# Optimization experiments

Hardware: AMD Instinct MI355X
Metric: run time of the kernel (lower is better)

Reference implementation:

```python
import jax, jax.numpy as jnp
import numpy as np

IN_FEATS = 64
ONSET = 0.8
CUTOFF = 1.0
N_NODES = 100000
N_EDGES = 1600000


def smooth_cutoff(d):
    # 1 below onset, 0 above cutoff, smooth cosine ramp in between
    x = (d - ONSET) / (CUTOFF - ONSET)
    ramp = 0.5 * (jnp.cos(jnp.pi * jnp.clip(x, 0.0, 1.0)) + 1.0)
    return jnp.where(d <= ONSET, 1.0, jnp.where(d >= CUTOFF, 0.0, ramp))


def setup_inputs() -> dict:
    key = jax.random.key(0)
    ks = jax.random.split(key, 8)
    h = jax.random.normal(ks[0], (N_NODES, IN_FEATS), dtype=jnp.float32)
    dist = jax.random.uniform(ks[1], (N_EDGES,), dtype=jnp.float32)
    W1 = jax.random.normal(ks[2], (IN_FEATS, IN_FEATS), dtype=jnp.float32) / jnp.sqrt(IN_FEATS)
    b1 = jnp.zeros((IN_FEATS,), dtype=jnp.float32)
    W2 = jax.random.normal(ks[3], (IN_FEATS, IN_FEATS), dtype=jnp.float32) / jnp.sqrt(IN_FEATS)
    b2 = jnp.zeros((IN_FEATS,), dtype=jnp.float32)
    src_idx = jax.random.randint(ks[4], (N_EDGES,), 0, N_NODES, dtype=jnp.int64 if jax.config.jax_enable_x64 else jnp.int32).astype(jnp.int32)
    dst_idx = jax.random.randint(ks[5], (N_EDGES,), 0, N_NODES, dtype=jnp.int32)
    return {"h": h, "dist": dist, "W1": W1, "b1": b1, "W2": W2, "b2": b2,
            "src_idx": src_idx, "dst_idx": dst_idx}


def reference(h, dist, W1, b1, W2, b2, src_idx, dst_idx):
    gamma = jnp.float32(IN_FEATS / (CUTOFF - 0.0))  # in_feats / (range hi - lo)
    muk = jnp.linspace(0.0, CUTOFF, IN_FEATS, dtype=jnp.float32)  # [K]
    # per-edge RBF basis: [E, K]
    rbf = jnp.exp(-gamma * (dist[:, None] - muk[None, :]) ** 2)
    fcut = smooth_cutoff(dist)[:, None]  # [E, 1]
    msg = h[src_idx] * rbf * fcut  # gather src feats, [E, K]
    agg = jax.ops.segment_sum(msg, dst_idx, num_segments=N_NODES)  # [N, K]
    # MLP: Linear -> softplus -> Linear
    hid = jax.nn.softplus(agg @ W1 + b1)
    out = hid @ W2 + b2
    return out
```

## Files before the change

kernel.cpp:

```cpp
#include <hip/hip_runtime.h>
#include <hip/hip_fp16.h>
#include <math.h>

#define IN_FEATS 64
#define N_NODES 100000
#define N_EDGES 1600000
#define BSHIFT 7
#define NPB 128
#define NBUCK ((N_NODES + NPB - 1) / NPB)
#define CAP 4088
#define PCHUNK 8192
#define PGRID ((N_EDGES + PCHUNK - 1) / PCHUNK)
#define NGRP (N_NODES / 16)

#define KSCALE 9.6089785f

typedef __attribute__((ext_vector_type(8))) short short8_t;
typedef __attribute__((ext_vector_type(4))) float f32x4_t;

#define MFMA16(a, b, c) __builtin_amdgcn_mfma_f32_16x16x32_bf16(a, b, c, 0, 0, 0)

__device__ __forceinline__ unsigned short bf16_rne(float x) {
    unsigned u = __float_as_uint(x);
    unsigned r = u + 0x7FFFu + ((u >> 16) & 1u);
    return (unsigned short)(r >> 16);
}

__device__ __forceinline__ short8_t u4_to_s8(uint4 v) {
    union { uint4 u; short8_t s; } cv; cv.u = v; return cv.s;
}

__device__ __forceinline__ void split8(float4 a, float4 b,
                                       short8_t* hi, short8_t* lo) {
    float x0 = a.x, x1 = a.y, x2 = a.z, x3 = a.w;
    float x4 = b.x, x5 = b.y, x6 = b.z, x7 = b.w;
    short8_t h, l;
#define SP(I, X) { unsigned short hu = bf16_rne(X); \
        float hf = __uint_as_float((unsigned)hu << 16); \
        unsigned short lu = bf16_rne((X) - hf); \
        h[I] = (short)hu; l[I] = (short)lu; }
    SP(0, x0) SP(1, x1) SP(2, x2) SP(3, x3)
    SP(4, x4) SP(5, x5) SP(6, x6) SP(7, x7)
#undef SP
    *hi = h; *lo = l;
}

__device__ __forceinline__ float edge_coef(float d, float mu) {
    float t = d - mu;
    float rbf = __expf(-64.0f * t * t);
    float x  = (d - 0.8f) * 5.0f;
    float xc = fminf(fmaxf(x, 0.0f), 1.0f);
    float ramp = 0.5f * (__cosf(3.14159265358979323846f * xc) + 1.0f);
    float fc = (d <= 0.8f) ? 1.0f : ((d >= 1.0f) ? 0.0f : ramp);
    return rbf * fc;
}

__device__ __forceinline__ float cutoff_fc(float d) {
    float x  = (d - 0.8f) * 5.0f;
    float xc = fminf(fmaxf(x, 0.0f), 1.0f);
    float ramp = 0.5f * (__cosf(3.14159265358979323846f * xc) + 1.0f);
    return (d <= 0.8f) ? 1.0f : ((d >= 1.0f) ? 0.0f : ramp);
}

__global__ __launch_bounds__(256) void init_kernel(int* __restrict__ bcursor,
                                                   int* __restrict__ offs,
                                                   const float* __restrict__ W1,
                                                   const float* __restrict__ W2,
                                                   uint4* __restrict__ wfrag) {
    int i = blockIdx.x * 256 + threadIdx.x;
    if (i < NBUCK) bcursor[i] = i * CAP;
    if (i == 0) offs[N_NODES] = N_EDGES;
    if (i < 2048) {
        int lane  = i & 63;
        int tile  = (i >> 6) & 7;
        int hl    = (i >> 9) & 1;
        int layer = (i >> 10) & 1;
        const float* W = layer ? W2 : W1;
        int kbase = (tile >> 2) * 32 + (lane >> 4) * 8;
        int j     = (tile & 3) * 16 + (lane & 15);
        unsigned p[4];
        #pragma unroll
        for (int e = 0; e < 8; e += 2) {
            float x0 = W[(kbase + e) * 64 + j];
            float x1 = W[(kbase + e + 1) * 64 + j];
            unsigned short u0, u1;
            if (hl == 0) {
                u0 = bf16_rne(x0);
                u1 = bf16_rne(x1);
            } else {
                unsigned short h0 = bf16_rne(x0);
                unsigned short h1 = bf16_rne(x1);
                u0 = bf16_rne(x0 - __uint_as_float((unsigned)h0 << 16));
                u1 = bf16_rne(x1 - __uint_as_float((unsigned)h1 << 16));
            }
            p[e >> 1] = (unsigned)u0 | ((unsigned)u1 << 16);
        }
        wfrag[i] = make_uint4(p[0], p[1], p[2], p[3]);
    }
}

__global__ __launch_bounds__(1024) void partition_kernel(const int* __restrict__ dst,
                                                         const int* __restrict__ src,
                                                         const float* __restrict__ dist,
                                                         int* __restrict__ bcursor,
                                                         int2* __restrict__ brec) {
    __shared__ int hist[NBUCK];
    __shared__ int base_[NBUCK];
    int tid = threadIdx.x;
    for (int i = tid; i < NBUCK; i += 1024) hist[i] = 0;
    __syncthreads();

    int e0 = blockIdx.x * PCHUNK;
    int e1 = min(e0 + PCHUNK, N_EDGES);

    for (int t = e0 + tid; t < e1; t += 1024)
        atomicAdd(&hist[dst[t] >> BSHIFT], 1);
    __syncthreads();

    for (int i = tid; i < NBUCK; i += 1024) {
        int hv = hist[i];
        if (hv) base_[i] = atomicAdd(&bcursor[i], hv);
        hist[i] = 0;
    }
    __syncthreads();

    for (int t = e0 + tid; t < e1; t += 1024) {
        int d  = dst[t];
        int b  = d >> BSHIFT;
        int r  = atomicAdd(&hist[b], 1);
        float dv = dist[t];
        float fc = cutoff_fc(dv);
        float lfc = (fc > 0.0f) ? __log2f(fc) : -512.0f;
        unsigned dq = (unsigned)(fminf(fmaxf(dv, 0.0f), 1.0f) * 65535.0f + 0.5f);
        unsigned hf = (unsigned)__half_as_ushort(__float2half(lfc));
        int2 rec;
        rec.x = src[t] | ((d & (NPB - 1)) << 17);
        rec.y = (int)((hf << 16) | dq);
        brec[(size_t)base_[b] + r] = rec;
    }
}

__global__ __launch_bounds__(1024) void bscan_kernel(const int* __restrict__ bcursor,
                                                     int* __restrict__ boffs) {
    __shared__ int lds[1024];
    int tid = threadIdx.x;
    int v = (tid < NBUCK) ? (bcursor[tid] - tid * CAP) : 0;
    lds[tid] = v;
    __syncthreads();
    for (int off = 1; off < 1024; off <<= 1) {
        int x = (tid >= off) ? lds[tid - off] : 0;
        __syncthreads();
        lds[tid] += x;
        __syncthreads();
    }
    if (tid < NBUCK) boffs[tid] = lds[tid] - v;
    if (tid == 0) boffs[NBUCK] = N_EDGES;
}

__global__ __launch_bounds__(256) void node_sort_kernel(const int2* __restrict__ brec,
                                                        const int* __restrict__ boffs,
                                                        int2* __restrict__ rec_sorted,
                                                        int* __restrict__ offs) {
    __shared__ int cntL[NPB];
    __shared__ int scanL[NPB];
    __shared__ int curL[NPB];

    int b   = blockIdx.x;
    int tid = threadIdx.x;
    int beg = boffs[b];
    int cnt = boffs[b + 1] - beg;
    size_t pbase = (size_t)b * CAP;
    int node0 = b << BSHIFT;

    for (int i = tid; i < NPB; i += 256) cntL[i] = 0;
    __syncthreads();

    for (int t = tid; t < cnt; t += 256)
        atomicAdd(&cntL[(brec[pbase + t].x >> 17) & (NPB - 1)], 1);
    __syncthreads();

    if (tid < NPB) scanL[tid] = cntL[tid];
    __syncthreads();
    for (int off = 1; off < NPB; off <<= 1) {
        int x = 0;
        if (tid < NPB && tid >= off) x = scanL[tid - off];
        __syncthreads();
        if (tid < NPB) scanL[tid] += x;
        __syncthreads();
    }
    if (tid < NPB) {
        int excl = scanL[tid] - cntL[tid];
        curL[tid] = excl;
        int node = node0 + tid;
        if (node < N_NODES) offs[node] = beg + excl;
    }
    __syncthreads();

    for (int t = tid; t < cnt; t += 256) {
        int2 r = brec[pbase + t];
        int dl = (r.x >> 17) & (NPB - 1);
        int p  = atomicAdd(&curL[dl], 1);
        rec_sorted[(size_t)beg + p] = r;
    }
}

__global__ __launch_bounds__(256) void agg_kernel(
    const float* __restrict__ h,
    const int* __restrict__ offs,
    const int2* __restrict__ rec_sorted,
    float* __restrict__ out)
{
    int w    = threadIdx.x >> 6;
    int lane = threadIdx.x & 63;
    int node = blockIdx.x * 4 + w;
    if (node >= N_NODES) return;

    int beg = __builtin_amdgcn_readfirstlane(offs[node]);
    int end = __builtin_amdgcn_readfirstlane(offs[node + 1]);
    float muK = (float)lane * (KSCALE / 63.0f);
    float acc0 = 0.0f, acc1 = 0.0f;

#define REC(J, ACC) { \
        int2 r_ = rec_sorted[(size_t)(J)]; \
        int rx_ = __builtin_amdgcn_readfirstlane(r_.x); \
        unsigned ry_ = (unsigned)__builtin_amdgcn_readfirstlane(r_.y); \
        float hv_ = h[((size_t)(rx_ & 0x1FFFF) << 6) + lane]; \
        float dqf_ = (float)(ry_ & 0xFFFFu); \
        float lfc_ = __half2float(__ushort_as_half((unsigned short)(ry_ >> 16))); \
        float t_  = fmaf(dqf_, (KSCALE / 65535.0f), -muK); \
        float a_  = fmaf(-t_, t_, lfc_); \
        ACC = fmaf(hv_, exp2f(a_), ACC); }

    int i = beg;
    int main_end = beg + ((end - beg) & ~7);
    for (; i < main_end; i += 8) {
        REC(i + 0, acc0) REC(i + 1, acc1) REC(i + 2, acc0) REC(i + 3, acc1)
        REC(i + 4, acc0) REC(i + 5, acc1) REC(i + 6, acc0) REC(i + 7, acc1)
    }
    for (; i < end; ++i) { REC(i, acc0) }
#undef REC

    out[(size_t)node * 64 + lane] = acc0 + acc1;
}

__global__ __launch_bounds__(256) void mlp_kernel(
    float* __restrict__ io, const uint4* __restrict__ wfrag,
    const float* __restrict__ b1, const float* __restrict__ b2)
{
    __shared__ float hidL[4][16][68];

    int tid  = threadIdx.x;
    int lane = tid & 63;
    int wv   = tid >> 6;
    int grp  = blockIdx.x * 4 + wv;
    if (grp >= NGRP) return;
    int node0 = grp * 16;
    int lrow = lane & 15, lk = lane >> 4;

    const float* arow = io + (size_t)(node0 + lrow) * 64 + lk * 8;
    float4 t0 = *(const float4*)(arow);
    float4 t1 = *(const float4*)(arow + 4);
    float4 t2 = *(const float4*)(arow + 32);
    float4 t3 = *(const float4*)(arow + 36);
    short8_t Ah0, Al0, Ah1, Al1;
    split8(t0, t1, &Ah0, &Al0);
    split8(t2, t3, &Ah1, &Al1);

    f32x4_t acc[4];
    #pragma unroll
    for (int n = 0; n < 4; ++n) {
        float b = b1[n * 16 + lrow];
        acc[n] = (f32x4_t){b, b, b, b};
    }
    #pragma unroll
    for (int n = 0; n < 4; ++n) {
        short8_t wh0 = u4_to_s8(wfrag[(n) * 64 + lane]);
        short8_t wh1 = u4_to_s8(wfrag[(4 + n) * 64 + lane]);
        short8_t wl0 = u4_to_s8(wfrag[512 + n * 64 + lane]);
        short8_t wl1 = u4_to_s8(wfrag[512 + (4 + n) * 64 + lane]);
        f32x4_t c = acc[n];
        c = MFMA16(Ah0, wh0, c);
        c = MFMA16(Ah1, wh1, c);
        c = MFMA16(Ah0, wl0, c);
        c = MFMA16(Ah1, wl1, c);
        c = MFMA16(Al0, wh0, c);
        c = MFMA16(Al1, wh1, c);
        acc[n] = c;
    }

    #pragma unroll
    for (int n = 0; n < 4; ++n) {
        #pragma unroll
        for (int r = 0; r < 4; ++r) {
            float v = acc[n][r];
            float e = exp2f(v * 1.44269504089f);
            float sp = 0.69314718056f * __log2f(1.0f + e);
            v = (v > 20.0f) ? v : sp;
            hidL[wv][lk * 4 + r][n * 16 + lrow] = v;
        }
    }
    __threadfence_block();

    const float* hrow = &hidL[wv][lrow][lk * 8];
    float4 h0 = *(const float4*)(hrow);
    float4 h1 = *(const float4*)(hrow + 4);
    float4 h2 = *(const float4*)(hrow + 32);
    float4 h3 = *(const float4*)(hrow + 36);
    short8_t Bh0, Bl0, Bh1, Bl1;
    split8(h0, h1, &Bh0, &Bl0);
    split8(h2, h3, &Bh1, &Bl1);

    f32x4_t oac[4];
    #pragma unroll
    for (int n = 0; n < 4; ++n) {
        float b = b2[n * 16 + lrow];
        oac[n] = (f32x4_t){b, b, b, b};
    }
    #pragma unroll
    for (int n = 0; n < 4; ++n) {
        short8_t wh0 = u4_to_s8(wfrag[1024 + n * 64 + lane]);
        short8_t wh1 = u4_to_s8(wfrag[1024 + (4 + n) * 64 + lane]);
        short8_t wl0 = u4_to_s8(wfrag[1536 + n * 64 + lane]);
        short8_t wl1 = u4_to_s8(wfrag[1536 + (4 + n) * 64 + lane]);
        f32x4_t c = oac[n];
        c = MFMA16(Bh0, wh0, c);
        c = MFMA16(Bh1, wh1, c);
        c = MFMA16(Bh0, wl0, c);
        c = MFMA16(Bh1, wl1, c);
        c = MFMA16(Bl0, wh0, c);
        c = MFMA16(Bl1, wh1, c);
        oac[n] = c;
    }

    #pragma unroll
    for (int n = 0; n < 4; ++n) {
        #pragma unroll
        for (int r = 0; r < 4; ++r) {
            io[(size_t)(node0 + lk * 4 + r) * 64 + n * 16 + lrow] = oac[n][r];
        }
    }
}

__global__ __launch_bounds__(256) void schnet_edge_kernel(
    const float* __restrict__ h,
    const float* __restrict__ dist,
    const int* __restrict__ src_idx,
    const int* __restrict__ dst_idx,
    float* __restrict__ agg)
{
    long long idx = (long long)blockIdx.x * 256 + threadIdx.x;
    int e = (int)(idx >> 6);
    if (e >= N_EDGES) return;
    int k = (int)(idx & 63);
    float d = dist[e];
    float c = edge_coef(d, (float)k * (1.0f / 63.0f));
    int s  = src_idx[e];
    int dn = dst_idx[e];
    atomicAdd(&agg[(long long)dn * 64 + k], h[(long long)s * 64 + k] * c);
}

__global__ __launch_bounds__(256) void mlp_fallback_kernel(
    float* __restrict__ io,
    const float* __restrict__ W1, const float* __restrict__ b1,
    const float* __restrict__ W2, const float* __restrict__ b2)
{
    __shared__ float sW1[64 * 64];
    __shared__ float sW2[64 * 64];
    __shared__ float sRow[4][64];
    __shared__ float sHid[4][64];
    int tid = threadIdx.x;
    for (int i = tid; i < 4096; i += 256) { sW1[i] = W1[i]; sW2[i] = W2[i]; }
    __syncthreads();
    int lane = tid & 63, w = tid >> 6;
    float bb1 = b1[lane], bb2 = b2[lane];
    for (int base = blockIdx.x * 4; base < N_NODES; base += gridDim.x * 4) {
        int node = base + w;
        if (node < N_NODES) sRow[w][lane] = io[(size_t)node * 64 + lane];
        __syncthreads();
        float a = bb1;
        #pragma unroll
        for (int k = 0; k < 64; ++k) a = fmaf(sRow[w][k], sW1[k * 64 + lane], a);
        sHid[w][lane] = (a > 20.f) ? a : log1pf(__expf(a));
        __syncthreads();
        float c = bb2;
        #pragma unroll
        for (int k = 0; k < 64; ++k) c = fmaf(sHid[w][k], sW2[k * 64 + lane], c);
        if (node < N_NODES) io[(size_t)node * 64 + lane] = c;
        __syncthreads();
    }
}

extern "C" void kernel_launch(void* const* d_in, const int* in_sizes, int n_in,
                              void* d_out, int out_size, void* d_ws, size_t ws_size,
                              hipStream_t stream) {
    const float* h    = (const float*)d_in[0];
    const float* dist = (const float*)d_in[1];
    const float* W1   = (const float*)d_in[2];
    const float* b1   = (const float*)d_in[3];
    const float* W2   = (const float*)d_in[4];
    const float* b2   = (const float*)d_in[5];
    const int* src    = (const int*)d_in[6];
    const int* dst    = (const int*)d_in[7];
    float* out        = (float*)d_out;

    size_t needed = ((size_t)2 * N_EDGES + NBUCK + 1 + NBUCK + N_NODES + 1 + 8192)
                    * sizeof(int);

    if (ws_size >= needed) {
        int2* rec_sorted = (int2*)d_ws;
        int* boffs       = (int*)d_ws + (size_t)2 * N_EDGES;
        int* bcursor     = boffs + NBUCK + 1;
        int* offs        = bcursor + NBUCK;
        uint4* wfrag     = (uint4*)(offs + N_NODES + 1);

        int2* brec = (int2*)d_out;

        init_kernel<<<16, 256, 0, stream>>>(bcursor, offs, W1, W2, wfrag);
        partition_kernel<<<PGRID, 1024, 0, stream>>>(dst, src, dist, bcursor, brec);
        bscan_kernel<<<1, 1024, 0, stream>>>(bcursor, boffs);
        node_sort_kernel<<<NBUCK, 256, 0, stream>>>(brec, boffs, rec_sorted, offs);
        agg_kernel<<<N_NODES / 4, 256, 0, stream>>>(h, offs, rec_sorted, out);
        mlp_kernel<<<(NGRP + 3) / 4, 256, 0, stream>>>(out, wfrag, b1, b2);
    } else {
        hipMemsetAsync(out, 0, (size_t)N_NODES * IN_FEATS * sizeof(float), stream);
        long long total = (long long)N_EDGES * 64;
        schnet_edge_kernel<<<(int)((total + 255) / 256), 256, 0, stream>>>(
            h, dist, src, dst, out);
        mlp_fallback_kernel<<<2048, 256, 0, stream>>>(out, W1, b1, W2, b2);
    }
}
```

Measured before the change: 124.4 us.

## Gather bf16 copy of node features in aggregation and stage bucket records in LDS

Adds a pre-pass that converts h to bf16 in workspace, plus a new aggregation kernel that gathers the 2-byte features instead of fp32, halving random-gather traffic. node_sort now caches bucket records in shared memory so it no longer reads them from global twice. The partition chunk size is doubled. The bf16 gather lowers the precision of the node features, and the extra conversion kernel and the larger LDS footprint add some cost.

```diff
diff --git a/kernel.cpp b/kernel.cpp
--- a/kernel.cpp
+++ b/kernel.cpp
@@ -9,7 +9,7 @@
 #define NPB 128
 #define NBUCK ((N_NODES + NPB - 1) / NPB)
 #define CAP 4088
-#define PCHUNK 8192
+#define PCHUNK 16384
 #define PGRID ((N_EDGES + PCHUNK - 1) / PCHUNK)
 #define NGRP (N_NODES / 16)
 
@@ -32,15 +32,13 @@
 
 __device__ __forceinline__ void split8(float4 a, float4 b,
                                        short8_t* hi, short8_t* lo) {
-    float x0 = a.x, x1 = a.y, x2 = a.z, x3 = a.w;
-    float x4 = b.x, x5 = b.y, x6 = b.z, x7 = b.w;
     short8_t h, l;
 #define SP(I, X) { unsigned short hu = bf16_rne(X); \
         float hf = __uint_as_float((unsigned)hu << 16); \
         unsigned short lu = bf16_rne((X) - hf); \
         h[I] = (short)hu; l[I] = (short)lu; }
-    SP(0, x0) SP(1, x1) SP(2, x2) SP(3, x3)
-    SP(4, x4) SP(5, x5) SP(6, x6) SP(7, x7)
+    SP(0, a.x) SP(1, a.y) SP(2, a.z) SP(3, a.w)
+    SP(4, b.x) SP(5, b.y) SP(6, b.z) SP(7, b.w)
 #undef SP
     *hi = h; *lo = l;
 }
@@ -99,6 +97,20 @@
     }
 }
 
+__global__ __launch_bounds__(256) void h2bf16_kernel(const float* __restrict__ h,
+                                                     unsigned short* __restrict__ hb) {
+    int i = blockIdx.x * 256 + threadIdx.x;
+    if (i < N_NODES * 8) {
+        const float4* p = (const float4*)(h + (size_t)i * 8);
+        float4 a = p[0], b = p[1];
+        unsigned u0 = (unsigned)bf16_rne(a.x) | ((unsigned)bf16_rne(a.y) << 16);
+        unsigned u1 = (unsigned)bf16_rne(a.z) | ((unsigned)bf16_rne(a.w) << 16);
+        unsigned u2 = (unsigned)bf16_rne(b.x) | ((unsigned)bf16_rne(b.y) << 16);
+        unsigned u3 = (unsigned)bf16_rne(b.z) | ((unsigned)bf16_rne(b.w) << 16);
+        *(uint4*)(hb + (size_t)i * 8) = make_uint4(u0, u1, u2, u3);
+    }
+}
+
 __global__ __launch_bounds__(1024) void partition_kernel(const int* __restrict__ dst,
                                                          const int* __restrict__ src,
                                                          const float* __restrict__ dist,
@@ -164,6 +176,7 @@
     __shared__ int cntL[NPB];
     __shared__ int scanL[NPB];
     __shared__ int curL[NPB];
+    __shared__ int2 stage[CAP];
 
     int b   = blockIdx.x;
     int tid = threadIdx.x;
@@ -175,8 +188,11 @@
     for (int i = tid; i < NPB; i += 256) cntL[i] = 0;
     __syncthreads();
 
-    for (int t = tid; t < cnt; t += 256)
-        atomicAdd(&cntL[(brec[pbase + t].x >> 17) & (NPB - 1)], 1);
+    for (int t = tid; t < cnt; t += 256) {
+        int2 r = brec[pbase + t];
+        stage[t] = r;
+        atomicAdd(&cntL[(r.x >> 17) & (NPB - 1)], 1);
+    }
     __syncthreads();
 
     if (tid < NPB) scanL[tid] = cntL[tid];
@@ -197,11 +213,51 @@
     __syncthreads();
 
     for (int t = tid; t < cnt; t += 256) {
-        int2 r = brec[pbase + t];
+        int2 r = stage[t];
         int dl = (r.x >> 17) & (NPB - 1);
         int p  = atomicAdd(&curL[dl], 1);
         rec_sorted[(size_t)beg + p] = r;
     }
+}
+
+__global__ __launch_bounds__(256) void agg_bf16_kernel(
+    const unsigned short* __restrict__ hb,
+    const int* __restrict__ offs,
+    const int2* __restrict__ rec_sorted,
+    float* __restrict__ out)
+{
+    int w    = threadIdx.x >> 6;
+    int lane = threadIdx.x & 63;
+    int node = blockIdx.x * 4 + w;
+    if (node >= N_NODES) return;
+
+    int beg = __builtin_amdgcn_readfirstlane(offs[node]);
+    int end = __builtin_amdgcn_readfirstlane(offs[node + 1]);
+    float muK = (float)lane * (KSCALE / 63.0f);
+    float acc0 = 0.0f, acc1 = 0.0f;
+
+#define REC(J, ACC) { \
+        int2 r_ = rec_sorted[(size_t)(J)]; \
+        int rx_ = __builtin_amdgcn_readfirstlane(r_.x); \
+        unsigned ry_ = (unsigned)__builtin_amdgcn_readfirstlane(r_.y); \
+        unsigned hvu_ = (unsigned)hb[((size_t)(rx_ & 0x1FFFF) << 6) + lane]; \
+        float hv_ = __uint_as_float(hvu_ << 16); \
+        float dqf_ = (float)(ry_ & 0xFFFFu); \
+        float lfc_ = __half2float(__ushort_as_half((unsigned short)(ry_ >> 16))); \
+        float t_  = fmaf(dqf_, (KSCALE / 65535.0f), -muK); \
+        float a_  = fmaf(-t_, t_, lfc_); \
+        ACC = fmaf(hv_, exp2f(a_), ACC); }
+
+    int i = beg;
+    int main_end = beg + ((end - beg) & ~7);
+    for (; i < main_end; i += 8) {
+        REC(i + 0, acc0) REC(i + 1, acc1) REC(i + 2, acc0) REC(i + 3, acc1)
+        REC(i + 4, acc0) REC(i + 5, acc1) REC(i + 6, acc0) REC(i + 7, acc1)
+    }
+    for (; i < end; ++i) { REC(i, acc0) }
+#undef REC
+
+    out[(size_t)node * 64 + lane] = acc0 + acc1;
 }
 
 __global__ __launch_bounds__(256) void agg_kernel(
@@ -403,23 +459,36 @@
     const int* dst    = (const int*)d_in[7];
     float* out        = (float*)d_out;
 
-    size_t needed = ((size_t)2 * N_EDGES + NBUCK + 1 + NBUCK + N_NODES + 1 + 8192)
-                    * sizeof(int);
-
-    if (ws_size >= needed) {
-        int2* rec_sorted = (int2*)d_ws;
-        int* boffs       = (int*)d_ws + (size_t)2 * N_EDGES;
-        int* bcursor     = boffs + NBUCK + 1;
-        int* offs        = bcursor + NBUCK;
-        uint4* wfrag     = (uint4*)(offs + N_NODES + 1);
+    const size_t WFRAG_B = 32768;
+    const size_t HB_B    = (size_t)N_NODES * 64 * 2;
+    const size_t RS_B    = (size_t)N_EDGES * 8;
+    const size_t INTS_B  = ((size_t)NBUCK + 1 + NBUCK + N_NODES + 1) * 4;
+    size_t need_f32  = WFRAG_B + RS_B + INTS_B;
+    size_t need_bf16 = WFRAG_B + HB_B + RS_B + INTS_B;
+
+    if (ws_size >= need_f32) {
+        bool use_bf16 = (ws_size >= need_bf16);
+        char* p = (char*)d_ws;
+        uint4* wfrag = (uint4*)p;              p += WFRAG_B;
+        unsigned short* hb = (unsigned short*)p;
+        if (use_bf16)                          p += HB_B;
+        int2* rec_sorted = (int2*)p;           p += RS_B;
+        int* boffs   = (int*)p;
+        int* bcursor = boffs + NBUCK + 1;
+        int* offs    = bcursor + NBUCK;
 
         int2* brec = (int2*)d_out;
 
         init_kernel<<<16, 256, 0, stream>>>(bcursor, offs, W1, W2, wfrag);
+        if (use_bf16)
+            h2bf16_kernel<<<(N_NODES * 8 + 255) / 256, 256, 0, stream>>>(h, hb);
         partition_kernel<<<PGRID, 1024, 0, stream>>>(dst, src, dist, bcursor, brec);
         bscan_kernel<<<1, 1024, 0, stream>>>(bcursor, boffs);
         node_sort_kernel<<<NBUCK, 256, 0, stream>>>(brec, boffs, rec_sorted, offs);
-        agg_kernel<<<N_NODES / 4, 256, 0, stream>>>(h, offs, rec_sorted, out);
+        if (use_bf16)
+            agg_bf16_kernel<<<N_NODES / 4, 256, 0, stream>>>(hb, offs, rec_sorted, out);
+        else
+            agg_kernel<<<N_NODES / 4, 256, 0, stream>>>(h, offs, rec_sorted, out);
         mlp_kernel<<<(NGRP + 3) / 4, 256, 0, stream>>>(out, wfrag, b1, b2);
     } else {
         hipMemsetAsync(out, 0, (size_t)N_NODES * IN_FEATS * sizeof(float), stream);
```

Result: slower. 129.2 us (+3.9%).
